# Kernel tuning notes

Measured on AMD Instinct MI355X. Metric: run time of the kernel, lower is better.

## Reference

```python
import jax, jax.numpy as jnp
import numpy as np

MO = 48          # max_output_len (positional slots)
D = 32           # d_inner
NA = 8           # n_actions
STOP = 0
CAT_PRIM, CAT_MOD, CAT_COMB = 0, 1, 2


def _mlp(feats, w1, b1, w2, b2, w3, b3):
    # Linear -> GELU(exact, erf) -> Linear -> GELU -> Linear (torch nn.GELU default is exact)
    h = jax.nn.gelu(feats @ w1.T + b1, approximate=False)
    h = jax.nn.gelu(h @ w2.T + b2, approximate=False)
    return h @ w3.T + b3


def setup_inputs() -> dict:
    key = jax.random.key(0)
    ks = jax.random.split(key, 20)
    B, N = 1024, 16
    inp = {
        'node_cats': jax.random.randint(ks[0], (B, N), 0, 3, dtype=jnp.int32),
        'node_subs': jax.random.randint(ks[1], (B, N), 0, 2, dtype=jnp.int32),
        'node_mask': jax.random.randint(ks[2], (B, N), 0, 2, dtype=jnp.int32),
        'child_left': jax.random.randint(ks[3], (B, N), 0, N, dtype=jnp.int32),
        'child_right': jax.random.randint(ks[4], (B, N), 0, N, dtype=jnp.int32),
        'action_embed': jax.random.normal(ks[5], (NA, D), jnp.float32),
        'mod_w1': jax.random.normal(ks[6], (128, 3), jnp.float32) * 0.1,
        'mod_b1': jax.random.normal(ks[7], (128,), jnp.float32) * 0.02,
        'mod_w2': jax.random.normal(ks[8], (128, 128), jnp.float32) * 0.05,
        'mod_b2': jax.random.normal(ks[9], (128,), jnp.float32) * 0.02,
        'mod_w3': jax.random.normal(ks[10], (MO * MO, 128), jnp.float32) * 0.01,
        'mod_b3': (4.0 * jnp.eye(MO)).flatten(),  # identity-ish init as in torch code
        'comb_w1': jax.random.normal(ks[11], (128, 4), jnp.float32) * 0.1,
        'comb_b1': jax.random.normal(ks[12], (128,), jnp.float32) * 0.02,
        'comb_w2': jax.random.normal(ks[13], (128, 128), jnp.float32) * 0.05,
        'comb_b2': jax.random.normal(ks[14], (128,), jnp.float32) * 0.02,
        'comb_w3': jax.random.normal(ks[15], (MO * 2 * MO, 128), jnp.float32) * 0.01,
        'comb_b3': (4.0 * jnp.eye(MO, 2 * MO)).flatten(),
    }
    return inp


def _forward(node_cats, node_subs, node_mask, child_left, child_right,
             action_embed, mod_w1, mod_b1, mod_w2, mod_b2, mod_w3, mod_b3,
             comb_w1, comb_b1, comb_w2, comb_b2, comb_w3, comb_b3):
    B, N = node_cats.shape
    mask = node_mask.astype(bool)
    cl = jnp.clip(child_left, 0, N - 1)
    cr = jnp.clip(child_right, 0, N - 1)
    prim_mask = (node_cats == CAT_PRIM) & mask
    mod_mask = (node_cats == CAT_MOD) & mask
    comb_mask = (node_cats == CAT_COMB) & mask
    subs01 = jnp.clip(node_subs, 0, 1)
    sub_oh = jax.nn.one_hot(subs01, 2, dtype=jnp.float32)  # (B,N,2)

    # --- primitive init: buffer[0] = action_embed[subs+1], zeros elsewhere ---
    action_ids = jnp.clip(node_subs + 1, 0, NA - 1)
    prim_vecs = action_embed[action_ids]  # (B,N,D)
    buffers = jnp.zeros((B, N, MO, D), jnp.float32)
    buffers = buffers.at[:, :, 0, :].set(prim_vecs * prim_mask[..., None].astype(jnp.float32))
    counts = prim_mask.astype(jnp.float32)  # (B,N)

    # --- modifier stage ---
    child_buf = jnp.take_along_axis(buffers, cl[:, :, None, None], axis=1)  # (B,N,MO,D)
    child_cnt = jnp.take_along_axis(counts, cl, axis=1)  # (B,N)
    feats = jnp.concatenate([child_cnt[..., None] / MO, sub_oh], axis=-1)  # (B,N,3)
    logits = _mlp(feats, mod_w1, mod_b1, mod_w2, mod_b2, mod_w3, mod_b3).reshape(B, N, MO, MO)
    attn = jax.nn.softmax(logits, axis=-1)
    mod_buf = jnp.einsum('bnpq,bnqd->bnpd', attn, child_buf)
    factors = jnp.array([2.0, 3.0], jnp.float32)[subs01]
    mod_cnt = jnp.minimum(child_cnt * factors, float(MO))
    buffers = jnp.where(mod_mask[:, :, None, None], mod_buf, buffers)
    counts = jnp.where(mod_mask, mod_cnt, counts)

    # --- combinator stage ---
    left_buf = jnp.take_along_axis(buffers, cl[:, :, None, None], axis=1)
    right_buf = jnp.take_along_axis(buffers, cr[:, :, None, None], axis=1)
    left_cnt = jnp.take_along_axis(counts, cl, axis=1)
    right_cnt = jnp.take_along_axis(counts, cr, axis=1)
    feats = jnp.concatenate([left_cnt[..., None] / MO, right_cnt[..., None] / MO, sub_oh], axis=-1)  # (B,N,4)
    logits = _mlp(feats, comb_w1, comb_b1, comb_w2, comb_b2, comb_w3, comb_b3).reshape(B, N, MO, 2 * MO)
    attn = jax.nn.softmax(logits, axis=-1)
    concat_buf = jnp.concatenate([left_buf, right_buf], axis=2)  # (B,N,2MO,D)
    comb_buf = jnp.einsum('bnpq,bnqd->bnpd', attn, concat_buf)
    comb_cnt = jnp.minimum(left_cnt + right_cnt, float(MO))
    buffers = jnp.where(comb_mask[:, :, None, None], comb_buf, buffers)
    counts = jnp.where(comb_mask, comb_cnt, counts)

    # --- decode root with tied embedding + stop bias ---
    root_buf = buffers[:, 0, :, :]  # (B,MO,D)
    out = jnp.einsum('bpd,ad->bpa', root_buf, action_embed)  # (B,MO,NA)
    positions = jnp.arange(MO, dtype=jnp.float32)[None, :]  # (1,MO)
    is_stop = (positions >= counts[:, 0:1]).astype(jnp.float32)[..., None]  # (B,MO,1)
    stop_bias = jnp.zeros((NA,), jnp.float32).at[STOP].set(8.0)
    return out + is_stop * stop_bias


def reference(node_cats, node_subs, node_mask, child_left, child_right,
              action_embed, mod_w1, mod_b1, mod_w2, mod_b2, mod_w3, mod_b3,
              comb_w1, comb_b1, comb_w2, comb_b2, comb_w3, comb_b3):
    return _forward(node_cats, node_subs, node_mask, child_left, child_right,
                    action_embed, mod_w1, mod_b1, mod_w2, mod_b2, mod_w3, mod_b3,
                    comb_w1, comb_b1, comb_w2, comb_b2, comb_w3, comb_b3)
```

## Files before the change

kernel.cpp:

```cpp
#include <hip/hip_runtime.h>
#include <hip/hip_bf16.h>
#include <float.h>


#define NNODE 16

#define MODCOL_OFF 0
#define G_OFF      192
#define ATT_OFF    256

__device__ __forceinline__ float gelu_exact(float x) {
    return 0.5f * x * (1.0f + erff(x * 0.70710678118654752f));
}

__device__ __forceinline__ float dot128(const float* __restrict__ w,
                                        const float* __restrict__ h) {
    const float4* w4 = (const float4*)w;
    float s = 0.f;
    #pragma unroll
    for (int i = 0; i < 32; ++i) {
        float4 v = w4[i];
        s += v.x * h[4 * i + 0] + v.y * h[4 * i + 1] +
             v.z * h[4 * i + 2] + v.w * h[4 * i + 3];
    }
    return s;
}

__global__ __launch_bounds__(128) void scan_tables(
    const float* __restrict__ E,
    const float* __restrict__ mw1, const float* __restrict__ mb1,
    const float* __restrict__ mw2, const float* __restrict__ mb2,
    const float* __restrict__ mw3, const float* __restrict__ mb3,
    const float* __restrict__ cw1, const float* __restrict__ cb1,
    const float* __restrict__ cw2, const float* __restrict__ cb2,
    const float* __restrict__ cw3, const float* __restrict__ cb3,
    float* __restrict__ ws)
{
    __shared__ float h1[128];
    __shared__ float h2s[128];
    __shared__ float lg[96];
    __shared__ float red[4];

    const int tid = threadIdx.x;
    const int blk = blockIdx.x;

    if (blk < 96) {
        const int mm = blk / 48, p = blk % 48;
        const float f0 = 1.0f / 48.0f;
        const float f1 = (mm == 0) ? 1.0f : 0.0f;
        const float f2 = (mm == 1) ? 1.0f : 0.0f;
        h1[tid] = gelu_exact(mw1[tid * 3 + 0] * f0 + mw1[tid * 3 + 1] * f1 +
                             mw1[tid * 3 + 2] * f2 + mb1[tid]);
        __syncthreads();
        h2s[tid] = gelu_exact(dot128(mw2 + tid * 128, h1) + mb2[tid]);
        __syncthreads();
        if (tid < 48)
            lg[tid] = dot128(mw3 + (p * 48 + tid) * 128, h2s) + mb3[p * 48 + tid];
        __syncthreads();
        if (tid == 0) {
            float mx = lg[0];
            for (int q = 1; q < 48; ++q) mx = fmaxf(mx, lg[q]);
            float s = 0.f;
            for (int q = 0; q < 48; ++q) s += expf(lg[q] - mx);
            ws[MODCOL_OFF + (2 + mm) * 48 + p] = expf(lg[0] - mx) / s;
        }
        return;
    }
    if (blk == 96) {
        if (tid < 64) {
            const int i = tid >> 3, a = tid & 7;
            float s = 0.f;
            #pragma unroll
            for (int d = 0; d < 32; ++d) s += E[i * 32 + d] * E[a * 32 + d];
            ws[G_OFF + tid] = s;
        }
        return;
    }

    const int u = blk - 97;
    const int p = u >> 5;
    const int c = u & 31;
    const int csub = c & 1;
    const int rc = (c >> 1) & 3;
    const int lc = (c >> 3) & 3;

    const float f0 = (float)lc / 48.0f;
    const float f1 = (float)rc / 48.0f;
    const float f2 = (csub == 0) ? 1.0f : 0.0f;
    const float f3 = (csub == 1) ? 1.0f : 0.0f;
    h1[tid] = gelu_exact(cw1[tid * 4 + 0] * f0 + cw1[tid * 4 + 1] * f1 +
                         cw1[tid * 4 + 2] * f2 + cw1[tid * 4 + 3] * f3 + cb1[tid]);
    __syncthreads();
    h2s[tid] = gelu_exact(dot128(cw2 + tid * 128, h1) + cb2[tid]);
    __syncthreads();

    const int j = tid & 3;
    const int rbase = tid >> 2;
    const float4* h24 = (const float4*)h2s;
    #pragma unroll
    for (int o = 0; o < 3; ++o) {
        const int r = o * 32 + rbase;
        const float4* w4 = (const float4*)(cw3 + (p * 96 + r) * 128);
        float s = 0.f;
        #pragma unroll
        for (int i = 0; i < 8; ++i) {
            const int f4i = i * 4 + j;
            float4 w = w4[f4i];
            float4 h = h24[f4i];
            s += w.x * h.x + w.y * h.y + w.z * h.z + w.w * h.w;
        }
        s += __shfl_xor(s, 1);
        s += __shfl_xor(s, 2);
        if (j == 0) lg[r] = s;
    }
    __syncthreads();

    const int wv = tid >> 6;
    float lv = (tid < 96) ? (lg[tid] + cb3[p * 96 + tid]) : -FLT_MAX;
    float m = lv;
    #pragma unroll
    for (int d = 32; d > 0; d >>= 1) m = fmaxf(m, __shfl_xor(m, d));
    if ((tid & 63) == 0) red[wv] = m;
    __syncthreads();
    const float mx = fmaxf(red[0], red[1]);

    float ev = (tid < 96) ? expf(lv - mx) : 0.f;
    float sum = ev;
    #pragma unroll
    for (int d = 32; d > 0; d >>= 1) sum += __shfl_xor(sum, d);
    if ((tid & 63) == 0) red[2 + wv] = sum;
    __syncthreads();
    const float inv = 1.0f / (red[2] + red[3]);

    if (tid < 96)
        ws[ATT_OFF + (c * 48 + p) * 96 + tid] = ev * inv;
}

__global__ __launch_bounds__(384) void scan_output(
    const int* __restrict__ cats, const int* __restrict__ subs,
    const int* __restrict__ mask, const int* __restrict__ cl,
    const int* __restrict__ cr,
    const float* __restrict__ ws,
    float* __restrict__ out)
{
    __shared__ int sc[NNODE], ss[NNODE], sm[NNODE], sl[NNODE], sr[NNODE];
    __shared__ int s_dec[11];
    __shared__ float s_G[64];
    __shared__ float s_mc[96];
    __shared__ float s_w[96];

    const int b = blockIdx.x;
    const int tid = threadIdx.x;
    if (tid < NNODE) {
        sc[tid] = cats[b * NNODE + tid];
        ss[tid] = subs[b * NNODE + tid];
        sm[tid] = mask[b * NNODE + tid];
        sl[tid] = cl[b * NNODE + tid];
        sr[tid] = cr[b * NNODE + tid];
    } else if (tid >= 96 && tid < 192) {
        s_mc[tid - 96] = ws[MODCOL_OFF + 96 + (tid - 96)];
    } else if (tid >= 192 && tid < 256) {
        s_G[tid - 192] = ws[G_OFF + tid - 192];
    }
    __syncthreads();

    if (tid == 0) {
        auto clampN  = [](int x) { return x < 0 ? 0 : (x > NNODE - 1 ? NNODE - 1 : x); };
        auto clamp01 = [](int x) { return x < 0 ? 0 : (x > 1 ? 1 : x); };
        auto clampA  = [](int x) { return x < 0 ? 0 : (x > 7 ? 7 : x); };
        auto PRIM = [&](int n) { return (sc[n] == 0) && (sm[n] != 0); };
        auto MODM = [&](int n) { return (sc[n] == 1) && (sm[n] != 0); };
        auto AID  = [&](int n) { return clampA(ss[n] + 1); };

        int modeL = 0, modeR = 0, baseL = 0, baseR = 0, strideL = 0, strideR = 0;
        int mselL = 0, mselR = 0, aidL = 0, aidR = 0, count0 = 0;
        const int  cat0 = sc[0];
        const bool msk0 = sm[0] != 0;
        const int  sub0 = clamp01(ss[0]);
        const int  cl0  = clampN(sl[0]);
        const int  cr0  = clampN(sr[0]);

        if (cat0 == 2 && msk0) {
            auto cnt2 = [&](int n) -> int {
                if (MODM(n)) {
                    int c1 = PRIM(clampN(sl[n])) ? 1 : 0;
                    int f  = clamp01(ss[n]) ? 3 : 2;
                    int v  = c1 * f;
                    return v > 48 ? 48 : v;
                }
                return PRIM(n) ? 1 : 0;
            };
            const int l = cl0, r = cr0;
            const int lcc = cnt2(l), rcc = cnt2(r);
            const int cidx = (lcc * 4 + rcc) * 2 + sub0;
            const int abase = ATT_OFF + cidx * 4608;
            count0 = lcc + rcc; if (count0 > 48) count0 = 48;
            if (MODM(l)) {
                const int g = clampN(sl[l]);
                if (PRIM(g)) {
                    modeL = 3; aidL = AID(g); mselL = clamp01(ss[l]);
                    baseL = abase;
                }
            } else if (PRIM(l)) {
                modeL = 1; aidL = AID(l);
                baseL = abase; strideL = 96;
            }
            if (MODM(r)) {
                const int g = clampN(sl[r]);
                if (PRIM(g)) {
                    modeR = 3; aidR = AID(g); mselR = clamp01(ss[r]);
                    baseR = abase + 48;
                }
            } else if (PRIM(r)) {
                modeR = 1; aidR = AID(r);
                baseR = abase + 48; strideR = 96;
            }
        } else if (cat0 == 1 && msk0) {
            const int ch = cl0;
            const int c1 = PRIM(ch) ? 1 : 0;
            count0 = c1 * (sub0 ? 3 : 2); if (count0 > 48) count0 = 48;
            if (c1) {
                modeL = 1; aidL = AID(ch);
                baseL = MODCOL_OFF + (2 + sub0) * 48; strideL = 1;
            }
        } else if (cat0 == 0 && msk0) {
            modeL = 2; aidL = AID(0); count0 = 1;
        }
        s_dec[0] = modeL;  s_dec[1] = modeR;
        s_dec[2] = baseL;  s_dec[3] = baseR;
        s_dec[4] = strideL; s_dec[5] = strideR;
        s_dec[6] = mselL;  s_dec[7] = mselR;
        s_dec[8] = aidL;   s_dec[9] = aidR;
        s_dec[10] = count0;
    }
    __syncthreads();

    if (tid < 96) {
        const int side = tid / 48;
        const int p = tid - side * 48;
        const int mode = s_dec[0 + side];
        const int base = s_dec[2 + side];
        float w = 0.f;
        if (mode == 1) {
            w = ws[base + p * s_dec[4 + side]];
        } else if (mode == 2) {
            w = (p == 0) ? 1.0f : 0.0f;
        } else if (mode == 3) {
            const float4* ar = (const float4*)(ws + base + p * 96);
            const float4* mr = (const float4*)(s_mc + s_dec[6 + side] * 48);
            float s = 0.f;
            #pragma unroll
            for (int q = 0; q < 12; ++q) {
                float4 a4 = ar[q], m4 = mr[q];
                s += a4.x * m4.x + a4.y * m4.y + a4.z * m4.z + a4.w * m4.w;
            }
            w = s;
        }
        s_w[tid] = w;
    }
    __syncthreads();

    const int p = tid >> 3, a = tid & 7;
    float v = s_w[p]      * s_G[s_dec[8] * 8 + a]
            + s_w[48 + p] * s_G[s_dec[9] * 8 + a];
    if (a == 0 && p >= s_dec[10]) v += 8.0f;
    out[b * 384 + tid] = v;
}

extern "C" void kernel_launch(void* const* d_in, const int* in_sizes, int n_in,
                              void* d_out, int out_size, void* d_ws, size_t ws_size,
                              hipStream_t stream) {
    const int* cats = (const int*)d_in[0];
    const int* subs = (const int*)d_in[1];
    const int* mask = (const int*)d_in[2];
    const int* cl   = (const int*)d_in[3];
    const int* cr   = (const int*)d_in[4];
    const float* E   = (const float*)d_in[5];
    const float* mw1 = (const float*)d_in[6];
    const float* mb1 = (const float*)d_in[7];
    const float* mw2 = (const float*)d_in[8];
    const float* mb2 = (const float*)d_in[9];
    const float* mw3 = (const float*)d_in[10];
    const float* mb3 = (const float*)d_in[11];
    const float* cw1 = (const float*)d_in[12];
    const float* cb1 = (const float*)d_in[13];
    const float* cw2 = (const float*)d_in[14];
    const float* cb2 = (const float*)d_in[15];
    const float* cw3 = (const float*)d_in[16];
    const float* cb3 = (const float*)d_in[17];
    float* ws  = (float*)d_ws;
    float* out = (float*)d_out;
    const int B = in_sizes[0] / NNODE;

    scan_tables<<<97 + 48 * 32, 128, 0, stream>>>(E, mw1, mb1, mw2, mb2, mw3, mb3,
                                                  cw1, cb1, cw2, cb2, cw3, cb3, ws);
    scan_output<<<B, 384, 0, stream>>>(cats, subs, mask, cl, cr, ws, out);
}
```

Before: 113.1 us.

## Transpose attention table layout for coalesced reads; parallelize mod softmax via wave shuffles

The precomputed attention table is now stored transposed (column-major per combination index), so each output position's weights are contiguous across threads in the scan kernel. Mode-1 and mode-3 reads become coalesced across p instead of strided by 96. The modifier-MLP softmax, which ran serially on one thread, now uses a 64-lane shuffle reduction. In exchange, the mode-3 dot product loses its float4 vectorization and the precompute writes become strided.

Result: no change. 112.5 us (-0.6%).

```diff
diff --git a/kernel.cpp b/kernel.cpp
--- a/kernel.cpp
+++ b/kernel.cpp
@@ -57,12 +57,17 @@
         if (tid < 48)
             lg[tid] = dot128(mw3 + (p * 48 + tid) * 128, h2s) + mb3[p * 48 + tid];
         __syncthreads();
-        if (tid == 0) {
-            float mx = lg[0];
-            for (int q = 1; q < 48; ++q) mx = fmaxf(mx, lg[q]);
-            float s = 0.f;
-            for (int q = 0; q < 48; ++q) s += expf(lg[q] - mx);
-            ws[MODCOL_OFF + (2 + mm) * 48 + p] = expf(lg[0] - mx) / s;
+        if (tid < 64) {
+            float lv = (tid < 48) ? lg[tid] : -FLT_MAX;
+            float mx = lv;
+            #pragma unroll
+            for (int d = 32; d > 0; d >>= 1) mx = fmaxf(mx, __shfl_xor(mx, d));
+            float ev = (tid < 48) ? expf(lv - mx) : 0.f;
+            float sm = ev;
+            #pragma unroll
+            for (int d = 32; d > 0; d >>= 1) sm += __shfl_xor(sm, d);
+            if (tid == 0)
+                ws[MODCOL_OFF + (2 + mm) * 48 + p] = ev / sm;
         }
         return;
     }
@@ -133,7 +138,7 @@
     const float inv = 1.0f / (red[2] + red[3]);
 
     if (tid < 96)
-        ws[ATT_OFF + (c * 48 + p) * 96 + tid] = ev * inv;
+        ws[ATT_OFF + c * 4608 + tid * 48 + p] = ev * inv;
 }
 
 __global__ __launch_bounds__(384) void scan_output(
@@ -144,7 +149,7 @@
     float* __restrict__ out)
 {
     __shared__ int sc[NNODE], ss[NNODE], sm[NNODE], sl[NNODE], sr[NNODE];
-    __shared__ int s_dec[11];
+    __shared__ int s_dec[9];
     __shared__ float s_G[64];
     __shared__ float s_mc[96];
     __shared__ float s_w[96];
@@ -172,7 +177,7 @@
         auto MODM = [&](int n) { return (sc[n] == 1) && (sm[n] != 0); };
         auto AID  = [&](int n) { return clampA(ss[n] + 1); };
 
-        int modeL = 0, modeR = 0, baseL = 0, baseR = 0, strideL = 0, strideR = 0;
+        int modeL = 0, modeR = 0, offL = 0, offR = 0;
         int mselL = 0, mselR = 0, aidL = 0, aidR = 0, count0 = 0;
         const int  cat0 = sc[0];
         const bool msk0 = sm[0] != 0;
@@ -199,21 +204,21 @@
                 const int g = clampN(sl[l]);
                 if (PRIM(g)) {
                     modeL = 3; aidL = AID(g); mselL = clamp01(ss[l]);
-                    baseL = abase;
+                    offL = abase;
                 }
             } else if (PRIM(l)) {
                 modeL = 1; aidL = AID(l);
-                baseL = abase; strideL = 96;
+                offL = abase;
             }
             if (MODM(r)) {
                 const int g = clampN(sl[r]);
                 if (PRIM(g)) {
                     modeR = 3; aidR = AID(g); mselR = clamp01(ss[r]);
-                    baseR = abase + 48;
+                    offR = abase + 48 * 48;
                 }
             } else if (PRIM(r)) {
                 modeR = 1; aidR = AID(r);
-                baseR = abase + 48; strideR = 96;
+                offR = abase + 48 * 48;
             }
         } else if (cat0 == 1 && msk0) {
             const int ch = cl0;
@@ -221,17 +226,14 @@
             count0 = c1 * (sub0 ? 3 : 2); if (count0 > 48) count0 = 48;
             if (c1) {
                 modeL = 1; aidL = AID(ch);
-                baseL = MODCOL_OFF + (2 + sub0) * 48; strideL = 1;
+                offL = MODCOL_OFF + (2 + sub0) * 48;
             }
         } else if (cat0 == 0 && msk0) {
             modeL = 2; aidL = AID(0); count0 = 1;
         }
-        s_dec[0] = modeL;  s_dec[1] = modeR;
-        s_dec[2] = baseL;  s_dec[3] = baseR;
-        s_dec[4] = strideL; s_dec[5] = strideR;
-        s_dec[6] = mselL;  s_dec[7] = mselR;
-        s_dec[8] = aidL;   s_dec[9] = aidR;
-        s_dec[10] = count0;
+        s_dec[0] = modeL; s_dec[1] = modeR; s_dec[2] = offL; s_dec[3] = offR;
+        s_dec[4] = mselL; s_dec[5] = mselR; s_dec[6] = aidL; s_dec[7] = aidR;
+        s_dec[8] = count0;
     }
     __syncthreads();
 
@@ -239,21 +241,18 @@
         const int side = tid / 48;
         const int p = tid - side * 48;
         const int mode = s_dec[0 + side];
-        const int base = s_dec[2 + side];
+        const int off  = s_dec[2 + side];
         float w = 0.f;
         if (mode == 1) {
-            w = ws[base + p * s_dec[4 + side]];
+            w = ws[off + p];
         } else if (mode == 2) {
             w = (p == 0) ? 1.0f : 0.0f;
         } else if (mode == 3) {
-            const float4* ar = (const float4*)(ws + base + p * 96);
-            const float4* mr = (const float4*)(s_mc + s_dec[6 + side] * 48);
+            const float* ar = ws + off + p;
+            const float* mr = s_mc + s_dec[4 + side] * 48;
             float s = 0.f;
             #pragma unroll
-            for (int q = 0; q < 12; ++q) {
-                float4 a4 = ar[q], m4 = mr[q];
-                s += a4.x * m4.x + a4.y * m4.y + a4.z * m4.z + a4.w * m4.w;
-            }
+            for (int q = 0; q < 48; ++q) s += ar[q * 48] * mr[q];
             w = s;
         }
         s_w[tid] = w;
@@ -261,9 +260,9 @@
     __syncthreads();
 
     const int p = tid >> 3, a = tid & 7;
-    float v = s_w[p]      * s_G[s_dec[8] * 8 + a]
-            + s_w[48 + p] * s_G[s_dec[9] * 8 + a];
-    if (a == 0 && p >= s_dec[10]) v += 8.0f;
+    float v = s_w[p]      * s_G[s_dec[6] * 8 + a]
+            + s_w[48 + p] * s_G[s_dec[7] * 8 + a];
+    if (a == 0 && p >= s_dec[8]) v += 8.0f;
     out[b * 384 + tid] = v;
 }
 
```
